# Kernel optimization log

Measured on AMD Instinct MI355X. Metric: run time of the kernel, lower is better.

The kernel has to match this reference:

```python
import jax, jax.numpy as jnp
import numpy as np

T, N, D, H = 1024, 8, 1024, 16
DK = D // H
NEG_INF = jnp.finfo(jnp.float32).min


def setup_inputs() -> dict:
    key = jax.random.key(0)
    ks = jax.random.split(key, 4)
    x = jax.random.normal(ks[0], (T, N, D), dtype=jnp.float32)
    # xavier-uniform-like scale for in_proj, small scale for w_o
    w_in = jax.random.normal(ks[1], (3 * D, D), dtype=jnp.float32) * 0.02
    b_in = jnp.zeros((3 * D,), dtype=jnp.float32)
    w_o = jax.random.normal(ks[2], (D, D), dtype=jnp.float32) * 0.02
    b_o = jnp.zeros((D,), dtype=jnp.float32)
    # causal mask: True = masked (score set to -inf)
    attn_mask = jnp.triu(jnp.ones((T, T), dtype=bool), k=1)
    # key padding: pad tail positions per batch element; True = padded
    lens = jnp.array([1024, 1000, 900, 800, 1024, 950, 700, 600], dtype=jnp.int32)
    key_padding_mask = jnp.arange(T)[None, :] >= lens[:, None]  # [N, S]
    return {"x": x, "w_in": w_in, "b_in": b_in, "w_o": w_o, "b_o": b_o,
            "attn_mask": attn_mask, "key_padding_mask": key_padding_mask}


def reference(x, w_in, b_in, w_o, b_o, attn_mask, key_padding_mask):
    # self-attention path: fused QKV projection, then chunk(3, dim=-1)
    qkv = jnp.einsum('tnd,ed->tne', x, w_in) + b_in  # [T, N, 3D]
    q, k, v = jnp.split(qkv, 3, axis=-1)
    # [T, N, D] -> [T, N, H, DK]
    q = q.reshape(T, N, H, DK)
    k = k.reshape(T, N, H, DK)
    v = v.reshape(T, N, H, DK)
    scale = 1.0 / jnp.sqrt(jnp.float32(DK))
    # score: [N, H, T, S]
    score = jnp.einsum('tnhd,snhd->nhts', q, k) * scale
    score = jnp.where(attn_mask[None, None, :, :], NEG_INF, score)
    score = jnp.where(key_padding_mask[:, None, None, :], NEG_INF, score)
    p = jax.nn.softmax(score, axis=-1)  # dropout p=0.0 -> identity
    out = jnp.einsum('nhts,snhd->tnhd', p, v).reshape(T, N, D)
    out = jnp.einsum('tnd,ed->tne', out, w_o) + b_o
    return out
```

## Files before the change

### kernel.cpp

```cpp
#include <hip/hip_runtime.h>


#define T_SEQ 1024
#define NB 8
#define DMODEL 1024
#define NHEADS 16
#define DK 64

typedef __attribute__((ext_vector_type(8))) short bf16x8;
typedef __attribute__((ext_vector_type(8))) unsigned short u16x8;
typedef __attribute__((ext_vector_type(4))) float f32x4;

#define MFMA16(a, b, c) __builtin_amdgcn_mfma_f32_16x16x32_bf16((a), (b), (c), 0, 0, 0)
#define WAITVM(N) asm volatile("s_waitcnt vmcnt(" #N ")" ::: "memory")

__device__ __forceinline__ unsigned short f2bf(float f) {
  unsigned int u = __float_as_uint(f);
  unsigned int r = (u + 0x7FFFu + ((u >> 16) & 1u)) >> 16;
  return (unsigned short)r;
}

__device__ __forceinline__ float fexp2(float x) {
  float r;
  asm("v_exp_f32 %0, %1" : "=v"(r) : "v"(x));
  return r;
}

__device__ __forceinline__ unsigned cvtpk(float lo, float hi) {
  unsigned r;
  asm("v_cvt_pk_bf16_f32 %0, %1, %2" : "=v"(r) : "v"(lo), "v"(hi));
  return r;
}

__device__ __forceinline__ void gload16(const void* g, void* l) {
  __builtin_amdgcn_global_load_lds((const __attribute__((address_space(1))) void*)g,
                                   (__attribute__((address_space(3))) void*)l, 16, 0, 0);
}

#define XQ (T_SEQ * NB * DMODEL / 4)
#define WIQ (3 * DMODEL * DMODEL / 4)
#define WOQ (DMODEL * DMODEL / 4)

__global__ __launch_bounds__(256) void cvt_all(const float* __restrict__ x,
                                               const float* __restrict__ w_in,
                                               const float* __restrict__ w_o,
                                               unsigned short* __restrict__ xb,
                                               unsigned short* __restrict__ wib,
                                               unsigned short* __restrict__ wob,
                                               const void* __restrict__ kpm_raw,
                                               int* __restrict__ lens) {
  int i = blockIdx.x * blockDim.x + threadIdx.x;
  if (blockIdx.x == 0 && threadIdx.x < 64) {
    const int* ki = (const int*)kpm_raw;
    const unsigned char* kb = (const unsigned char*)kpm_raw;
    const int lane = threadIdx.x;
    int bad = 0;
    for (int j = lane; j < 2048; j += 64) {
      unsigned v = (unsigned)ki[j];
      bad |= (v != 0u && v != 1u && v != 0x3F800000u) ? 1 : 0;
    }
    for (int m = 1; m < 64; m <<= 1) bad |= __shfl_xor(bad, m);
    for (int n = 0; n < NB; ++n) {
      int cnt = 0;
      if (bad) {
        for (int s = lane; s < T_SEQ; s += 64) cnt += (kb[n * T_SEQ + s] == 0) ? 1 : 0;
      } else {
        for (int s = lane; s < T_SEQ; s += 64) cnt += (ki[n * T_SEQ + s] == 0) ? 1 : 0;
      }
      for (int m = 1; m < 64; m <<= 1) cnt += __shfl_xor(cnt, m);
      if (lane == 0) lens[n] = cnt;
    }
  }
  const float* src;
  unsigned short* dst;
  int j;
  if (i < XQ) {
    src = x; dst = xb; j = i;
  } else if (i < XQ + WIQ) {
    src = w_in; dst = wib; j = i - XQ;
  } else if (i < XQ + WIQ + WOQ) {
    src = w_o; dst = wob; j = i - XQ - WIQ;
  } else {
    return;
  }
  float4 v = reinterpret_cast<const float4*>(src)[j];
  uint2 o;
  o.x = (unsigned)f2bf(v.x) | ((unsigned)f2bf(v.y) << 16);
  o.y = (unsigned)f2bf(v.z) | ((unsigned)f2bf(v.w) << 16);
  reinterpret_cast<uint2*>(dst)[j] = o;
}

#define QSCALE 0.18033688f

__global__ __launch_bounds__(256, 2) void gemm_qkv_wide(
    const unsigned short* __restrict__ A, const unsigned short* __restrict__ B,
    const float* __restrict__ bias, unsigned short* __restrict__ qb,
    unsigned short* __restrict__ kb, unsigned short* __restrict__ vtb) {
  constexpr int K = DMODEL;
  __shared__ unsigned short lds_all[2 * 12288];
  const int tid = threadIdx.x;
  const int brow = blockIdx.x * 256;
  const int bcol = blockIdx.y * 128;
  const int w = tid >> 6, lane = tid & 63;
  const int l15 = lane & 15, lg = lane >> 4;
  const int wm = w >> 1, wn = w & 1;

  f32x4 acc[8][4] = {};
  const int KT = K >> 5;

  auto stage = [&](int t, int buf) {
    const int k0 = t << 5;
    unsigned short* la = lds_all + buf * 12288;
    unsigned short* lb = la + 8192;
#pragma unroll
    for (int i = 0; i < 4; ++i) {
      const int seg = i * 256 + tid;
      const int row = seg >> 2, slot = seg & 3;
      const int qq = (slot ^ ((row >> 1) & 3)) * 8;
      gload16(A + (size_t)(brow + row) * K + k0 + qq, la + seg * 8);
    }
#pragma unroll
    for (int i = 0; i < 2; ++i) {
      const int seg = i * 256 + tid;
      const int row = seg >> 2, slot = seg & 3;
      const int qq = (slot ^ ((row >> 1) & 3)) * 8;
      gload16(B + (size_t)(bcol + row) * K + k0 + qq, lb + seg * 8);
    }
  };

  stage(0, 0);
  for (int t = 0; t < KT; ++t) {
    const int cur = t & 1;
    if (t + 1 < KT) {
      stage(t + 1, cur ^ 1);
      WAITVM(6);
    } else {
      WAITVM(0);
    }
    __builtin_amdgcn_s_barrier();

    const unsigned short* la = lds_all + cur * 12288;
    const unsigned short* lb = la + 8192;
    bf16x8 bfr[4];
#pragma unroll
    for (int ni = 0; ni < 4; ++ni) {
      const int row = wn * 64 + ni * 16 + l15;
      bfr[ni] = *reinterpret_cast<const bf16x8*>(lb + row * 32 +
                                                 ((lg ^ ((row >> 1) & 3)) << 3));
    }
#pragma unroll
    for (int mi = 0; mi < 8; ++mi) {
      const int row = wm * 128 + mi * 16 + l15;
      const bf16x8 af = *reinterpret_cast<const bf16x8*>(la + row * 32 +
                                                         ((lg ^ ((row >> 1) & 3)) << 3));
#pragma unroll
      for (int ni = 0; ni < 4; ++ni) acc[mi][ni] = MFMA16(af, bfr[ni], acc[mi][ni]);
    }
    __builtin_amdgcn_s_barrier();
  }

  if (bcol >= 2 * DMODEL) {
    unsigned short* tl = lds_all;
    const int t0 = brow >> 3;
#pragma unroll
    for (int pass = 0; pass < 2; ++pass) {
      if (wn == pass) {
#pragma unroll
        for (int ni = 0; ni < 4; ++ni) {
          const int c = ni * 16 + l15;
          const float bv = bias[bcol + pass * 64 + c];
#pragma unroll
          for (int mi = 0; mi < 8; ++mi) {
#pragma unroll
            for (int r = 0; r < 4; ++r) {
              const int row = wm * 128 + mi * 16 + lg * 4 + r;
              const int tloc = row >> 3, nn = row & 7;
              tl[c * 276 + nn * 32 + tloc] = f2bf(acc[mi][ni][r] + bv);
            }
          }
        }
      }
      __syncthreads();
      const int hh = ((bcol + pass * 64) - 2 * DMODEL) >> 6;
#pragma unroll
      for (int it = 0; it < 2; ++it) {
        const int task = it * 256 + tid;
        const int c = task >> 3, nn = task & 7;
        const unsigned short* sp = &tl[c * 276 + nn * 32];
        unsigned short* dst = vtb + (size_t)(nn * NHEADS + hh) * (T_SEQ * DK) +
                              (size_t)c * T_SEQ + t0;
#pragma unroll
        for (int q = 0; q < 4; ++q)
          *reinterpret_cast<u16x8*>(dst + q * 8) = *reinterpret_cast<const u16x8*>(sp + q * 8);
      }
      __syncthreads();
    }
    return;
  }

#pragma unroll
  for (int ni = 0; ni < 4; ++ni) {
    const int col = bcol + wn * 64 + ni * 16 + l15;
    const float bv = bias[col];
    unsigned short* basep = col < DMODEL ? qb : kb;
    const float scl = col < DMODEL ? QSCALE : 1.0f;
    const int c2 = col & (DMODEL - 1);
    const int hh = c2 >> 6, dk = c2 & 63;
#pragma unroll
    for (int mi = 0; mi < 8; ++mi) {
#pragma unroll
      for (int r = 0; r < 4; ++r) {
        const int row = brow + wm * 128 + mi * 16 + lg * 4 + r;
        const float v = (acc[mi][ni][r] + bv) * scl;
        const int t = row >> 3, n = row & 7;
        basep[(size_t)(n * NHEADS + hh) * (T_SEQ * DK) + t * DK + dk] = f2bf(v);
      }
    }
  }
}

__global__ __launch_bounds__(256) void gemm_out_kernel(
    const unsigned short* __restrict__ A, const unsigned short* __restrict__ B,
    const float* __restrict__ bias, float* __restrict__ Cf, int M, int N, int K) {
  __shared__ unsigned short lds_all[2 * 8192];
  const int tid = threadIdx.x;
  const int brow = blockIdx.x * 128;
  const int bcol = blockIdx.y * 128;
  const int w = tid >> 6, lane = tid & 63;
  const int l15 = lane & 15, lg = lane >> 4;
  const int wr = (w >> 1) * 64, wc = (w & 1) * 64;

  f32x4 acc[4][4] = {};
  const int KT = K >> 5;

  auto stage = [&](int t, int buf) {
    const int k0 = t << 5;
    unsigned short* la = lds_all + buf * 8192;
    unsigned short* lb = la + 4096;
#pragma unroll
    for (int i = 0; i < 2; ++i) {
      const int seg = i * 256 + tid;
      const int row = seg >> 2, slot = seg & 3;
      const int qq = (slot ^ ((row >> 1) & 3)) * 8;
      gload16(A + (size_t)(brow + row) * K + k0 + qq, la + seg * 8);
      gload16(B + (size_t)(bcol + row) * K + k0 + qq, lb + seg * 8);
    }
  };

  stage(0, 0);
  for (int t = 0; t < KT; ++t) {
    const int cur = t & 1;
    if (t + 1 < KT) {
      stage(t + 1, cur ^ 1);
      WAITVM(4);
    } else {
      WAITVM(0);
    }
    __builtin_amdgcn_s_barrier();

    const unsigned short* la = lds_all + cur * 8192;
    const unsigned short* lb = la + 4096;
    bf16x8 af[4], bfr[4];
#pragma unroll
    for (int mi = 0; mi < 4; ++mi) {
      const int row = wr + mi * 16 + l15;
      af[mi] = *reinterpret_cast<const bf16x8*>(la + row * 32 +
                                                ((lg ^ ((row >> 1) & 3)) << 3));
    }
#pragma unroll
    for (int ni = 0; ni < 4; ++ni) {
      const int row = wc + ni * 16 + l15;
      bfr[ni] = *reinterpret_cast<const bf16x8*>(lb + row * 32 +
                                                 ((lg ^ ((row >> 1) & 3)) << 3));
    }
#pragma unroll
    for (int mi = 0; mi < 4; ++mi)
#pragma unroll
      for (int ni = 0; ni < 4; ++ni)
        acc[mi][ni] = MFMA16(af[mi], bfr[ni], acc[mi][ni]);
    __builtin_amdgcn_s_barrier();
  }

#pragma unroll
  for (int mi = 0; mi < 4; ++mi) {
#pragma unroll
    for (int ni = 0; ni < 4; ++ni) {
      const int col = bcol + wc + ni * 16 + l15;
      const float bv = bias[col];
#pragma unroll
      for (int r = 0; r < 4; ++r) {
        const int row = brow + wr + mi * 16 + lg * 4 + r;
        Cf[(size_t)row * N + col] = acc[mi][ni][r] + bv;
      }
    }
  }
}

#define PLD 72

__device__ __forceinline__ void stage_kv(const unsigned short* kp_base,
                                         const unsigned short* vp_base, int s0,
                                         unsigned short* kl, unsigned short* vl, int tid) {
#pragma unroll
  for (int i = 0; i < 2; ++i) {
    const int seg = i * 256 + tid;
    const int r = seg >> 3, c8 = seg & 7;
    const int xc = (c8 ^ (r & 7)) * 8;
    gload16(kp_base + (((size_t)(s0 + r)) << 6) + xc, kl + seg * 8);
    gload16(vp_base + (size_t)r * T_SEQ + s0 + xc, vl + seg * 8);
  }
}

__global__ __launch_bounds__(256, 3) void attn_kernel(
    const unsigned short* __restrict__ qb, const unsigned short* __restrict__ kb,
    const unsigned short* __restrict__ vtb, const int* __restrict__ lens,
    unsigned short* __restrict__ attn_out) {
  __shared__ unsigned short k_lds[2][64 * 64];
  __shared__ unsigned short v_lds[2][64 * 64];
  __shared__ unsigned short p_lds[4 * 16 * PLD];
  const int bid = blockIdx.x;
  const int x = bid & 7;
  const int rem = bid >> 3;
  const int nh = (rem & 15) * 8 + x;
  const int pr = rem >> 4;
  const int n = nh >> 4;
  const int h = nh & 15;
  const int tid = threadIdx.x;
  const int w = tid >> 6, lane = tid & 63;
  const int l15 = lane & 15, lg = lane >> 4;
  const int len_n = lens[n];
  const int ltiles = (len_n + 63) >> 6;

  const unsigned short* kp_base = kb + (size_t)nh * (T_SEQ * DK);
  const unsigned short* vp_base = vtb + (size_t)nh * (T_SEQ * DK);
  const unsigned short* q_base = qb + (size_t)nh * (T_SEQ * DK);
  unsigned short* pw = p_lds + w * 16 * PLD;

  bf16x8 ones;
#pragma unroll
  for (int j = 0; j < 8; ++j) ones[j] = (short)0x3F80;

  const int qtA = pr, qtB = 15 - pr;
  int nA = qtA + 1, nB = qtB + 1;
  if (ltiles < nA) nA = ltiles;
  if (ltiles < nB) nB = ltiles;

  const unsigned short* qpA = q_base + (size_t)(qtA * 64 + w * 16 + l15) * DK;
  const unsigned short* qpB = q_base + (size_t)(qtB * 64 + w * 16 + l15) * DK;
  const bf16x8 qaA0 = *reinterpret_cast<const bf16x8*>(qpA + lg * 8);
  const bf16x8 qaA1 = *reinterpret_cast<const bf16x8*>(qpA + 32 + lg * 8);
  const bf16x8 qaB0 = *reinterpret_cast<const bf16x8*>(qpB + lg * 8);
  const bf16x8 qaB1 = *reinterpret_cast<const bf16x8*>(qpB + 32 + lg * 8);

  f32x4 oA[4] = {}, oB[4] = {};
  float lA[4] = {}, lB[4] = {};

  const int tbA = qtA * 64 + w * 16 + lg * 4;
  const int tbB = qtB * 64 + w * 16 + lg * 4;
  const int tlaneA = qtA * 64 + w * 16 + l15;
  const int tlaneB = qtB * 64 + w * 16 + l15;

  int cur = 0;
  stage_kv(kp_base, vp_base, 0, k_lds[0], v_lds[0], tid);

  for (int tile = 0; tile < nB; ++tile) {
    const int s0 = tile * 64;
    if (tile + 1 < nB) {
      stage_kv(kp_base, vp_base, s0 + 64, k_lds[cur ^ 1], v_lds[cur ^ 1], tid);
      WAITVM(4);
    } else {
      WAITVM(0);
    }
    __builtin_amdgcn_s_barrier();

    const bool actA = tile < nA;

    f32x4 sA[4] = {}, sB[4] = {};
    __builtin_amdgcn_s_setprio(1);
#pragma unroll
    for (int ct = 0; ct < 4; ++ct) {
      const int rl = ct * 16 + l15;
      const int c0 = lg ^ (rl & 7);
      const bf16x8 kf0 = *reinterpret_cast<const bf16x8*>(&k_lds[cur][rl * 64 + c0 * 8]);
      const bf16x8 kf1 = *reinterpret_cast<const bf16x8*>(&k_lds[cur][rl * 64 + (c0 ^ 4) * 8]);
      if (actA) {
        sA[ct] = MFMA16(kf0, qaA0, sA[ct]);
        sA[ct] = MFMA16(kf1, qaA1, sA[ct]);
      }
      sB[ct] = MFMA16(kf0, qaB0, sB[ct]);
      sB[ct] = MFMA16(kf1, qaB1, sB[ct]);
    }
    __builtin_amdgcn_s_setprio(0);
    bf16x8 vf[4][2];
#pragma unroll
    for (int ct = 0; ct < 4; ++ct) {
      const int rl = ct * 16 + l15;
      const int c0 = lg ^ (rl & 7);
      vf[ct][0] = *reinterpret_cast<const bf16x8*>(&v_lds[cur][rl * 64 + c0 * 8]);
      vf[ct][1] = *reinterpret_cast<const bf16x8*>(&v_lds[cur][rl * 64 + (c0 ^ 4) * 8]);
    }
    const int boundary = ((tile + 1) << 6) > len_n;

    if (actA) {
      if ((tile == qtA) | boundary) {
#pragma unroll
        for (int ct = 0; ct < 4; ++ct) {
          const int sb = s0 + ct * 16 + lg * 4;
#pragma unroll
          for (int r = 0; r < 4; ++r)
            if (sb + r > tlaneA || sb + r >= len_n) sA[ct][r] = -1e30f;
        }
      }
#pragma unroll
      for (int ct = 0; ct < 4; ++ct) {
        uint2 pk;
        pk.x = cvtpk(fexp2(sA[ct][0]), fexp2(sA[ct][1]));
        pk.y = cvtpk(fexp2(sA[ct][2]), fexp2(sA[ct][3]));
        *reinterpret_cast<uint2*>(pw + l15 * PLD + ct * 16 + lg * 4) = pk;
      }
      const bf16x8 pa0 = *reinterpret_cast<const bf16x8*>(pw + l15 * PLD + lg * 8);
      const bf16x8 pa1 = *reinterpret_cast<const bf16x8*>(pw + l15 * PLD + 32 + lg * 8);
      f32x4 lacc = {};
      __builtin_amdgcn_s_setprio(1);
      lacc = MFMA16(pa0, ones, lacc);
      lacc = MFMA16(pa1, ones, lacc);
#pragma unroll
      for (int ct = 0; ct < 4; ++ct) {
        oA[ct] = MFMA16(pa0, vf[ct][0], oA[ct]);
        oA[ct] = MFMA16(pa1, vf[ct][1], oA[ct]);
      }
      __builtin_amdgcn_s_setprio(0);
#pragma unroll
      for (int r = 0; r < 4; ++r) lA[r] += lacc[r];
    }

    {
      if ((tile == qtB) | boundary) {
#pragma unroll
        for (int ct = 0; ct < 4; ++ct) {
          const int sb = s0 + ct * 16 + lg * 4;
#pragma unroll
          for (int r = 0; r < 4; ++r)
            if (sb + r > tlaneB || sb + r >= len_n) sB[ct][r] = -1e30f;
        }
      }
#pragma unroll
      for (int ct = 0; ct < 4; ++ct) {
        uint2 pk;
        pk.x = cvtpk(fexp2(sB[ct][0]), fexp2(sB[ct][1]));
        pk.y = cvtpk(fexp2(sB[ct][2]), fexp2(sB[ct][3]));
        *reinterpret_cast<uint2*>(pw + l15 * PLD + ct * 16 + lg * 4) = pk;
      }
      const bf16x8 pa0 = *reinterpret_cast<const bf16x8*>(pw + l15 * PLD + lg * 8);
      const bf16x8 pa1 = *reinterpret_cast<const bf16x8*>(pw + l15 * PLD + 32 + lg * 8);
      f32x4 lacc = {};
      __builtin_amdgcn_s_setprio(1);
      lacc = MFMA16(pa0, ones, lacc);
      lacc = MFMA16(pa1, ones, lacc);
#pragma unroll
      for (int ct = 0; ct < 4; ++ct) {
        oB[ct] = MFMA16(pa0, vf[ct][0], oB[ct]);
        oB[ct] = MFMA16(pa1, vf[ct][1], oB[ct]);
      }
      __builtin_amdgcn_s_setprio(0);
#pragma unroll
      for (int r = 0; r < 4; ++r) lB[r] += lacc[r];
    }

    __builtin_amdgcn_s_barrier();
    cur ^= 1;
  }

#pragma unroll
  for (int r = 0; r < 4; ++r) { lA[r] = 1.0f / lA[r]; lB[r] = 1.0f / lB[r]; }
#pragma unroll
  for (int ct = 0; ct < 4; ++ct) {
    const int d = h * DK + ct * 16 + l15;
#pragma unroll
    for (int r = 0; r < 4; ++r) {
      attn_out[((size_t)(tbA + r) * NB + n) * DMODEL + d] = f2bf(oA[ct][r] * lA[r]);
      attn_out[((size_t)(tbB + r) * NB + n) * DMODEL + d] = f2bf(oB[ct][r] * lB[r]);
    }
  }
}

extern "C" void kernel_launch(void* const* d_in, const int* in_sizes, int n_in,
                              void* d_out, int out_size, void* d_ws, size_t ws_size,
                              hipStream_t stream) {
  const float* x = (const float*)d_in[0];
  const float* w_in = (const float*)d_in[1];
  const float* b_in = (const float*)d_in[2];
  const float* w_o = (const float*)d_in[3];
  const float* b_o = (const float*)d_in[4];
  const void* kpm = (const void*)d_in[6];
  float* out = (float*)d_out;

  char* ws = (char*)d_ws;
  unsigned short* x_bf = (unsigned short*)(ws + 0);
  unsigned short* win_bf = (unsigned short*)(ws + 16777216);
  unsigned short* wo_bf = (unsigned short*)(ws + 23068672);
  unsigned short* qb = (unsigned short*)(ws + 25165824);
  unsigned short* kb = (unsigned short*)(ws + 41943040);
  unsigned short* vtb = (unsigned short*)(ws + 58720256);
  unsigned short* attn_bf = (unsigned short*)(ws + 0);
  int* lens = (int*)(ws + 92274688);

  cvt_all<<<(XQ + WIQ + WOQ + 255) / 256, 256, 0, stream>>>(x, w_in, w_o, x_bf, win_bf, wo_bf,
                                                            kpm, lens);
  gemm_qkv_wide<<<dim3(32, 24), 256, 0, stream>>>(x_bf, win_bf, b_in, qb, kb, vtb);
  attn_kernel<<<NB * NHEADS * 8, 256, 0, stream>>>(qb, kb, vtb, lens, attn_bf);
  gemm_out_kernel<<<dim3(64, 8), 256, 0, stream>>>(attn_bf, wo_bf, b_o, out, T_SEQ * NB, DMODEL,
                                                   DMODEL);
}
```

Measured before the change: 142.4 us.

## Fuse fp32-to-bf16 conversion of x into QKV GEMM A-tile loading

Drops the separate conversion of the activation x to bf16. The QKV GEMM now loads fp32 x into registers, converts it with packed bf16 instructions and writes it to LDS, while B tiles still use direct global-to-LDS loads. The tile shrinks from 256x128 to 128x128 with occupancy hint 4 and the V-transpose epilogue is adapted to match. This removes a full write and reread of the 16 MB bf16 copy of x, but each A tile now moves twice as many bytes from global memory and goes through registers before reaching LDS.

```diff
diff --git a/kernel.cpp b/kernel.cpp
--- a/kernel.cpp
+++ b/kernel.cpp
@@ -13,6 +13,9 @@
 
 #define MFMA16(a, b, c) __builtin_amdgcn_mfma_f32_16x16x32_bf16((a), (b), (c), 0, 0, 0)
 #define WAITVM(N) asm volatile("s_waitcnt vmcnt(" #N ")" ::: "memory")
+#define LGKM0_FENCE                                  \
+  asm volatile("s_waitcnt lgkmcnt(0)" ::: "memory"); \
+  __builtin_amdgcn_sched_barrier(0)
 
 __device__ __forceinline__ unsigned short f2bf(float f) {
   unsigned int u = __float_as_uint(f);
@@ -37,18 +40,15 @@
                                    (__attribute__((address_space(3))) void*)l, 16, 0, 0);
 }
 
-#define XQ (T_SEQ * NB * DMODEL / 4)
 #define WIQ (3 * DMODEL * DMODEL / 4)
 #define WOQ (DMODEL * DMODEL / 4)
 
-__global__ __launch_bounds__(256) void cvt_all(const float* __restrict__ x,
-                                               const float* __restrict__ w_in,
-                                               const float* __restrict__ w_o,
-                                               unsigned short* __restrict__ xb,
-                                               unsigned short* __restrict__ wib,
-                                               unsigned short* __restrict__ wob,
-                                               const void* __restrict__ kpm_raw,
-                                               int* __restrict__ lens) {
+__global__ __launch_bounds__(256) void cvt_w(const float* __restrict__ w_in,
+                                             const float* __restrict__ w_o,
+                                             unsigned short* __restrict__ wib,
+                                             unsigned short* __restrict__ wob,
+                                             const void* __restrict__ kpm_raw,
+                                             int* __restrict__ lens) {
   int i = blockIdx.x * blockDim.x + threadIdx.x;
   if (blockIdx.x == 0 && threadIdx.x < 64) {
     const int* ki = (const int*)kpm_raw;
@@ -74,12 +74,10 @@
   const float* src;
   unsigned short* dst;
   int j;
-  if (i < XQ) {
-    src = x; dst = xb; j = i;
-  } else if (i < XQ + WIQ) {
-    src = w_in; dst = wib; j = i - XQ;
-  } else if (i < XQ + WIQ + WOQ) {
-    src = w_o; dst = wob; j = i - XQ - WIQ;
+  if (i < WIQ) {
+    src = w_in; dst = wib; j = i;
+  } else if (i < WIQ + WOQ) {
+    src = w_o; dst = wob; j = i - WIQ;
   } else {
     return;
   }
@@ -92,33 +90,49 @@
 
 #define QSCALE 0.18033688f
 
-__global__ __launch_bounds__(256, 2) void gemm_qkv_wide(
-    const unsigned short* __restrict__ A, const unsigned short* __restrict__ B,
+__global__ __launch_bounds__(256, 4) void gemm_qkv(
+    const float* __restrict__ X, const unsigned short* __restrict__ B,
     const float* __restrict__ bias, unsigned short* __restrict__ qb,
     unsigned short* __restrict__ kb, unsigned short* __restrict__ vtb) {
   constexpr int K = DMODEL;
-  __shared__ unsigned short lds_all[2 * 12288];
+  __shared__ unsigned short lds_all[2 * 8192];
   const int tid = threadIdx.x;
-  const int brow = blockIdx.x * 256;
+  const int brow = blockIdx.x * 128;
   const int bcol = blockIdx.y * 128;
   const int w = tid >> 6, lane = tid & 63;
   const int l15 = lane & 15, lg = lane >> 4;
-  const int wm = w >> 1, wn = w & 1;
-
-  f32x4 acc[8][4] = {};
+  const int wr = (w >> 1) * 64, wc = (w & 1) * 64;
+
+  f32x4 acc[4][4] = {};
   const int KT = K >> 5;
 
-  auto stage = [&](int t, int buf) {
+  const int rowA0 = tid >> 2, slotA0 = tid & 3;
+  const int qqA0 = (slotA0 ^ ((rowA0 >> 1) & 3)) * 8;
+  const int rowA1 = (256 + tid) >> 2, slotA1 = tid & 3;
+  const int qqA1 = (slotA1 ^ ((rowA1 >> 1) & 3)) * 8;
+  const float* xr0 = X + (size_t)(brow + rowA0) * K + qqA0;
+  const float* xr1 = X + (size_t)(brow + rowA1) * K + qqA1;
+
+  auto issueA = [&](int t, float4* f) {
     const int k0 = t << 5;
-    unsigned short* la = lds_all + buf * 12288;
-    unsigned short* lb = la + 8192;
-#pragma unroll
-    for (int i = 0; i < 4; ++i) {
-      const int seg = i * 256 + tid;
-      const int row = seg >> 2, slot = seg & 3;
-      const int qq = (slot ^ ((row >> 1) & 3)) * 8;
-      gload16(A + (size_t)(brow + row) * K + k0 + qq, la + seg * 8);
-    }
+    f[0] = *reinterpret_cast<const float4*>(xr0 + k0);
+    f[1] = *reinterpret_cast<const float4*>(xr0 + k0 + 4);
+    f[2] = *reinterpret_cast<const float4*>(xr1 + k0);
+    f[3] = *reinterpret_cast<const float4*>(xr1 + k0 + 4);
+  };
+  auto writeA = [&](int buf, const float4* f) {
+    unsigned short* la = lds_all + buf * 8192;
+    uint2 c0, c1;
+    c0.x = cvtpk(f[0].x, f[0].y); c0.y = cvtpk(f[0].z, f[0].w);
+    c1.x = cvtpk(f[1].x, f[1].y); c1.y = cvtpk(f[1].z, f[1].w);
+    *reinterpret_cast<uint4*>(la + tid * 8) = make_uint4(c0.x, c0.y, c1.x, c1.y);
+    c0.x = cvtpk(f[2].x, f[2].y); c0.y = cvtpk(f[2].z, f[2].w);
+    c1.x = cvtpk(f[3].x, f[3].y); c1.y = cvtpk(f[3].z, f[3].w);
+    *reinterpret_cast<uint4*>(la + (256 + tid) * 8) = make_uint4(c0.x, c0.y, c1.x, c1.y);
+  };
+  auto stageB = [&](int t, int buf) {
+    const int k0 = t << 5;
+    unsigned short* lb = lds_all + buf * 8192 + 4096;
 #pragma unroll
     for (int i = 0; i < 2; ++i) {
       const int seg = i * 256 + tid;
@@ -128,33 +142,49 @@
     }
   };
 
-  stage(0, 0);
+  float4 fA[4];
+  issueA(0, fA);
+  stageB(0, 0);
+  WAITVM(2);
+  writeA(0, fA);
+  LGKM0_FENCE;
+
   for (int t = 0; t < KT; ++t) {
     const int cur = t & 1;
     if (t + 1 < KT) {
-      stage(t + 1, cur ^ 1);
+      issueA(t + 1, fA);
+      stageB(t + 1, cur ^ 1);
       WAITVM(6);
     } else {
       WAITVM(0);
     }
     __builtin_amdgcn_s_barrier();
 
-    const unsigned short* la = lds_all + cur * 12288;
-    const unsigned short* lb = la + 8192;
-    bf16x8 bfr[4];
+    const unsigned short* la = lds_all + cur * 8192;
+    const unsigned short* lb = la + 4096;
+    bf16x8 af[4], bfr[4];
+#pragma unroll
+    for (int mi = 0; mi < 4; ++mi) {
+      const int row = wr + mi * 16 + l15;
+      af[mi] = *reinterpret_cast<const bf16x8*>(la + row * 32 +
+                                                ((lg ^ ((row >> 1) & 3)) << 3));
+    }
 #pragma unroll
     for (int ni = 0; ni < 4; ++ni) {
-      const int row = wn * 64 + ni * 16 + l15;
+      const int row = wc + ni * 16 + l15;
       bfr[ni] = *reinterpret_cast<const bf16x8*>(lb + row * 32 +
                                                  ((lg ^ ((row >> 1) & 3)) << 3));
     }
 #pragma unroll
-    for (int mi = 0; mi < 8; ++mi) {
-      const int row = wm * 128 + mi * 16 + l15;
-      const bf16x8 af = *reinterpret_cast<const bf16x8*>(la + row * 32 +
-                                                         ((lg ^ ((row >> 1) & 3)) << 3));
-#pragma unroll
-      for (int ni = 0; ni < 4; ++ni) acc[mi][ni] = MFMA16(af, bfr[ni], acc[mi][ni]);
+    for (int mi = 0; mi < 4; ++mi)
+#pragma unroll
+      for (int ni = 0; ni < 4; ++ni)
+        acc[mi][ni] = MFMA16(af[mi], bfr[ni], acc[mi][ni]);
+
+    if (t + 1 < KT) {
+      WAITVM(2);
+      writeA(cur ^ 1, fA);
+      LGKM0_FENCE;
     }
     __builtin_amdgcn_s_barrier();
   }
@@ -164,18 +194,18 @@
     const int t0 = brow >> 3;
 #pragma unroll
     for (int pass = 0; pass < 2; ++pass) {
-      if (wn == pass) {
+      if ((w & 1) == pass) {
 #pragma unroll
         for (int ni = 0; ni < 4; ++ni) {
           const int c = ni * 16 + l15;
-          const float bv = bias[bcol + pass * 64 + c];
-#pragma unroll
-          for (int mi = 0; mi < 8; ++mi) {
+          const float bv = bias[bcol + wc + ni * 16 + l15];
+#pragma unroll
+          for (int mi = 0; mi < 4; ++mi) {
 #pragma unroll
             for (int r = 0; r < 4; ++r) {
-              const int row = wm * 128 + mi * 16 + lg * 4 + r;
+              const int row = wr + mi * 16 + lg * 4 + r;
               const int tloc = row >> 3, nn = row & 7;
-              tl[c * 276 + nn * 32 + tloc] = f2bf(acc[mi][ni][r] + bv);
+              tl[c * 136 + nn * 16 + tloc] = f2bf(acc[mi][ni][r] + bv);
             }
           }
         }
@@ -186,12 +216,13 @@
       for (int it = 0; it < 2; ++it) {
         const int task = it * 256 + tid;
         const int c = task >> 3, nn = task & 7;
-        const unsigned short* sp = &tl[c * 276 + nn * 32];
+        const unsigned short* sp = &tl[c * 136 + nn * 16];
+        const u16x8 lo = *reinterpret_cast<const u16x8*>(sp);
+        const u16x8 hi = *reinterpret_cast<const u16x8*>(sp + 8);
         unsigned short* dst = vtb + (size_t)(nn * NHEADS + hh) * (T_SEQ * DK) +
                               (size_t)c * T_SEQ + t0;
-#pragma unroll
-        for (int q = 0; q < 4; ++q)
-          *reinterpret_cast<u16x8*>(dst + q * 8) = *reinterpret_cast<const u16x8*>(sp + q * 8);
+        *reinterpret_cast<u16x8*>(dst) = lo;
+        *reinterpret_cast<u16x8*>(dst + 8) = hi;
       }
       __syncthreads();
     }
@@ -199,18 +230,18 @@
   }
 
 #pragma unroll
-  for (int ni = 0; ni < 4; ++ni) {
-    const int col = bcol + wn * 64 + ni * 16 + l15;
-    const float bv = bias[col];
-    unsigned short* basep = col < DMODEL ? qb : kb;
-    const float scl = col < DMODEL ? QSCALE : 1.0f;
-    const int c2 = col & (DMODEL - 1);
-    const int hh = c2 >> 6, dk = c2 & 63;
-#pragma unroll
-    for (int mi = 0; mi < 8; ++mi) {
+  for (int mi = 0; mi < 4; ++mi) {
+#pragma unroll
+    for (int ni = 0; ni < 4; ++ni) {
+      const int col = bcol + wc + ni * 16 + l15;
+      const float bv = bias[col];
+      unsigned short* basep = col < DMODEL ? qb : kb;
+      const float scl = col < DMODEL ? QSCALE : 1.0f;
+      const int c2 = col & (DMODEL - 1);
+      const int hh = c2 >> 6, dk = c2 & 63;
 #pragma unroll
       for (int r = 0; r < 4; ++r) {
-        const int row = brow + wm * 128 + mi * 16 + lg * 4 + r;
+        const int row = brow + wr + mi * 16 + lg * 4 + r;
         const float v = (acc[mi][ni][r] + bv) * scl;
         const int t = row >> 3, n = row & 7;
         basep[(size_t)(n * NHEADS + hh) * (T_SEQ * DK) + t * DK + dk] = f2bf(v);
@@ -496,7 +527,6 @@
   float* out = (float*)d_out;
 
   char* ws = (char*)d_ws;
-  unsigned short* x_bf = (unsigned short*)(ws + 0);
   unsigned short* win_bf = (unsigned short*)(ws + 16777216);
   unsigned short* wo_bf = (unsigned short*)(ws + 23068672);
   unsigned short* qb = (unsigned short*)(ws + 25165824);
@@ -505,9 +535,8 @@
   unsigned short* attn_bf = (unsigned short*)(ws + 0);
   int* lens = (int*)(ws + 92274688);
 
-  cvt_all<<<(XQ + WIQ + WOQ + 255) / 256, 256, 0, stream>>>(x, w_in, w_o, x_bf, win_bf, wo_bf,
-                                                            kpm, lens);
-  gemm_qkv_wide<<<dim3(32, 24), 256, 0, stream>>>(x_bf, win_bf, b_in, qb, kb, vtb);
+  cvt_w<<<(WIQ + WOQ + 255) / 256, 256, 0, stream>>>(w_in, w_o, win_bf, wo_bf, kpm, lens);
+  gemm_qkv<<<dim3(64, 24), 256, 0, stream>>>(x, win_bf, b_in, qb, kb, vtb);
   attn_kernel<<<NB * NHEADS * 8, 256, 0, stream>>>(qb, kb, vtb, lens, attn_bf);
   gemm_out_kernel<<<dim3(64, 8), 256, 0, stream>>>(attn_bf, wo_bf, b_o, out, T_SEQ * NB, DMODEL,
                                                    DMODEL);
```

New measurement: 154.3 us. 1.08x slower.
